# Kernel optimization log

Measured on AMD Instinct MI355X. Metric: run time of the kernel, lower is better.

The kernel has to match this reference:

```python
import jax, jax.numpy as jnp
import numpy as np

CUTOFF = 5.0
NLINKED = 1
CELL_LIST = CUTOFF / NLINKED  # linked-cell edge length
_r = np.arange(-NLINKED, NLINKED + 1)
# torch.cartesian_prod(r1,r1,r1) == meshgrid(indexing='ij') stacked & flattened
LINKED = np.stack(np.meshgrid(_r, _r, _r, indexing='ij'), axis=-1).reshape(1, -1, 3).astype(np.float32)  # (1, 27, 3)


def setup_inputs() -> dict:
    N = 2744
    L = 30.0
    key = jax.random.key(0)
    k1, k2 = jax.random.split(key)
    coordinates = jax.random.uniform(k1, (N, 3), dtype=jnp.float32) * L
    cell = jnp.eye(3, dtype=jnp.float32) * L
    mass = jax.random.uniform(k2, (N,), dtype=jnp.float32) * 15.0 + 1.0
    period_table = jnp.ones((3,), dtype=jnp.int32)  # fully periodic
    return {"period_table": period_table, "coordinates": coordinates, "cell": cell, "mass": mass}


def _forward(period_table, coordinates, cell, mass):
    numatom = coordinates.shape[0]
    # wrap coordinates into the cell relative to atom 0 (fractional coords)
    inv_cell = jnp.linalg.inv(cell)
    inv_coor = coordinates @ inv_cell
    inv_coor = inv_coor - jnp.round(inv_coor - inv_coor[0])
    coordinates = inv_coor @ cell
    # remove center of mass
    com = (mass @ coordinates) / jnp.sum(mass)
    coordinates = coordinates - com[None, :]
    # periodic replicas needed to cover the cutoff
    num_repeats = jnp.ceil(jnp.min(CUTOFF / jnp.abs(cell), axis=0)).astype(jnp.int32)
    num_repeats = period_table.astype(jnp.int32) * num_repeats
    up = num_repeats + 1
    down = -num_repeats
    rs = [jnp.arange(int(down[i]), int(up[i])) for i in range(3)]
    g = jnp.meshgrid(*rs, indexing='ij')
    shifts_frac = jnp.stack(g, axis=-1).reshape(-1, 3).astype(coordinates.dtype)  # (S, 3)
    shifts = shifts_frac @ cell  # (S, 3) cartesian shift vectors
    num_shifts = shifts.shape[0]
    # prod = cartesian_prod(all_shifts, all_atoms).T : row0 shift idx, row1 atom idx
    prod0 = jnp.repeat(jnp.arange(num_shifts), numatom)
    prod1 = jnp.tile(jnp.arange(numatom), num_shifts)
    # shift box so all coords are positive; pad by cutoff
    mincoor = jnp.min(coordinates, axis=0) - CUTOFF - 1e-6
    coordinates = coordinates - mincoor
    maxcoor = jnp.max(coordinates, axis=0) + CUTOFF
    # all periodic images, keep only those inside the padded box
    image = (coordinates[None, :, :] + shifts[:, None, :]).reshape(-1, 3)
    keep = jnp.nonzero(((image < maxcoor) & (image > 0)).all(axis=1))[0]
    image_mask = image[keep]                      # (M, 3)
    prod0 = prod0[keep]
    prod1 = prod1[keep]
    # linked-cell indices
    ori_image_index = jnp.floor(coordinates / CELL_LIST)         # (N, 3)
    neigh_cell = ori_image_index[:, None, :] + jnp.asarray(LINKED)  # (N, 27, 3)
    image_index = jnp.floor(image_mask / CELL_LIST)              # (M, 3)
    max_cell_index = jnp.ceil(maxcoor / CELL_LIST)
    f10 = max_cell_index[1] * max_cell_index[0]
    neigh_cell_index = neigh_cell[:, :, 2] * f10 + neigh_cell[:, :, 1] * max_cell_index[0] + neigh_cell[:, :, 0]  # (N, 27)
    nimage_index = image_index[:, 2] * f10 + image_index[:, 1] * max_cell_index[0] + image_index[:, 0]            # (M,)
    # dense (N, M, 27) cell-index equality -- the memory-bound hot spot
    eq = neigh_cell_index[:, None, :] == nimage_index[None, :, None]
    ai, aj, _ = jnp.nonzero(eq)
    # distance filter on candidate pairs
    d = jnp.linalg.norm(coordinates[ai] - image_mask[aj], axis=-1)
    pair = jnp.nonzero((d < CUTOFF) & (d > 0.001))[0]
    center = ai[pair]
    img = aj[pair]
    shift_idx = prod0[img]
    atom_j = prod1[img]
    neigh_list = jnp.stack([center, atom_j])  # (2, P)
    return neigh_list, shifts[shift_idx], shifts_frac, shift_idx


def reference(period_table, coordinates, cell, mass):
    neigh_list, shifts_out, _, _ = _forward(period_table, coordinates, cell, mass)
    return (neigh_list, shifts_out)
```

## Files before the change

### kernel.cpp

```cpp
#include <hip/hip_runtime.h>
#include <math.h>

#define S_CAP     27
#define NCELL_MAX 4096
#define CAP       64
#define CAPSH     6
#define MAXNB     128
#define CUT       5.0f


__global__ __launch_bounds__(256)
void k1_pre(const int* __restrict__ period, const float* __restrict__ coor,
            const float* __restrict__ cell, const float* __restrict__ mass,
            int* hdr_i, float* hdr_f, float* shifts, float* xv,
            int* __restrict__ ccur, int n)
{
    #pragma clang fp contract(off)
    __shared__ double rs[256 * 4];
    __shared__ float  redf[256 * 6];
    __shared__ float  s_com[3];
    int t = threadIdx.x;

    for (int c = t; c < NCELL_MAX; c += 256) ccur[c] = 0;

    float c[3][3];
    #pragma unroll
    for (int i = 0; i < 3; i++)
        #pragma unroll
        for (int j = 0; j < 3; j++) c[i][j] = cell[3 * i + j];

    float a00 = c[1][1]*c[2][2] - c[1][2]*c[2][1];
    float a01 = c[0][2]*c[2][1] - c[0][1]*c[2][2];
    float a02 = c[0][1]*c[1][2] - c[0][2]*c[1][1];
    float a10 = c[1][2]*c[2][0] - c[1][0]*c[2][2];
    float a11 = c[0][0]*c[2][2] - c[0][2]*c[2][0];
    float a12 = c[0][2]*c[1][0] - c[0][0]*c[1][2];
    float a20 = c[1][0]*c[2][1] - c[1][1]*c[2][0];
    float a21 = c[0][1]*c[2][0] - c[0][0]*c[2][1];
    float a22 = c[0][0]*c[1][1] - c[0][1]*c[1][0];
    float det = c[0][0]*a00 + c[0][1]*a10 + c[0][2]*a20;
    float inv[3][3] = {{a00/det, a01/det, a02/det},
                       {a10/det, a11/det, a12/det},
                       {a20/det, a21/det, a22/det}};

    float f0[3];
    #pragma unroll
    for (int d = 0; d < 3; d++)
        f0[d] = coor[0]*inv[0][d] + coor[1]*inv[1][d] + coor[2]*inv[2][d];

    double sm = 0.0, sx = 0.0, sy = 0.0, sz = 0.0;
    for (int i = t; i < n; i += 256) {
        float p0 = coor[3*i], p1 = coor[3*i+1], p2 = coor[3*i+2];
        float ic[3], w[3], x[3];
        #pragma unroll
        for (int d = 0; d < 3; d++)
            ic[d] = p0*inv[0][d] + p1*inv[1][d] + p2*inv[2][d];
        #pragma unroll
        for (int d = 0; d < 3; d++)
            w[d] = ic[d] - rintf(ic[d] - f0[d]);
        #pragma unroll
        for (int d = 0; d < 3; d++)
            x[d] = w[0]*c[0][d] + w[1]*c[1][d] + w[2]*c[2][d];
        xv[3*i] = x[0]; xv[3*i+1] = x[1]; xv[3*i+2] = x[2];
        float m = mass[i];
        sm += (double)m;
        sx += (double)m * (double)x[0];
        sy += (double)m * (double)x[1];
        sz += (double)m * (double)x[2];
    }
    rs[t] = sm; rs[256+t] = sx; rs[512+t] = sy; rs[768+t] = sz;
    __syncthreads();
    for (int off = 128; off > 0; off >>= 1) {
        if (t < off) {
            rs[t]     += rs[t+off];
            rs[256+t] += rs[256+t+off];
            rs[512+t] += rs[512+t+off];
            rs[768+t] += rs[768+t+off];
        }
        __syncthreads();
    }
    if (t == 0) {
        float den = (float)rs[0];
        s_com[0] = ((float)rs[256]) / den;
        s_com[1] = ((float)rs[512]) / den;
        s_com[2] = ((float)rs[768]) / den;
    }
    __syncthreads();
    float com0 = s_com[0], com1 = s_com[1], com2 = s_com[2];

    float mn0 =  __builtin_inff(), mn1 =  __builtin_inff(), mn2 =  __builtin_inff();
    float mx0 = -__builtin_inff(), mx1 = -__builtin_inff(), mx2 = -__builtin_inff();
    for (int i = t; i < n; i += 256) {
        float v0 = xv[3*i]   - com0;
        float v1 = xv[3*i+1] - com1;
        float v2 = xv[3*i+2] - com2;
        xv[3*i] = v0; xv[3*i+1] = v1; xv[3*i+2] = v2;
        mn0 = fminf(mn0, v0); mn1 = fminf(mn1, v1); mn2 = fminf(mn2, v2);
        mx0 = fmaxf(mx0, v0); mx1 = fmaxf(mx1, v1); mx2 = fmaxf(mx2, v2);
    }
    redf[t]       = mn0; redf[256+t]  = mn1; redf[512+t]  = mn2;
    redf[768+t]   = mx0; redf[1024+t] = mx1; redf[1280+t] = mx2;
    __syncthreads();
    for (int off = 128; off > 0; off >>= 1) {
        if (t < off) {
            redf[t]      = fminf(redf[t],      redf[t+off]);
            redf[256+t]  = fminf(redf[256+t],  redf[256+t+off]);
            redf[512+t]  = fminf(redf[512+t],  redf[512+t+off]);
            redf[768+t]  = fmaxf(redf[768+t],  redf[768+t+off]);
            redf[1024+t] = fmaxf(redf[1024+t], redf[1024+t+off]);
            redf[1280+t] = fmaxf(redf[1280+t], redf[1280+t+off]);
        }
        __syncthreads();
    }
    if (t == 0) {
        float m20 = (redf[0]   - CUT) - 1e-6f;
        float m21 = (redf[256] - CUT) - 1e-6f;
        float m22 = (redf[512] - CUT) - 1e-6f;
        float maxc0 = (redf[768]  - m20) + CUT;
        float maxc1 = (redf[1024] - m21) + CUT;
        float maxc2 = (redf[1280] - m22) + CUT;
        float mcell0 = ceilf(maxc0 / CUT);
        float mcell1 = ceilf(maxc1 / CUT);
        float f10 = mcell1 * mcell0;
        int nr[3];
        for (int j = 0; j < 3; j++) {
            float v = __builtin_inff();
            for (int i = 0; i < 3; i++) {
                float q = CUT / fabsf(c[i][j]);
                v = fminf(v, q);
            }
            nr[j] = (int)ceilf(v);
            nr[j] *= period[j];
        }
        int nsz0 = 2*nr[0]+1, nsz1 = 2*nr[1]+1, nsz2 = 2*nr[2]+1;
        int S = nsz0 * nsz1 * nsz2;
        if (S > S_CAP) S = S_CAP;
        hdr_i[0] = S;
        hdr_i[3] = -nr[0]; hdr_i[4] = -nr[1]; hdr_i[5] = -nr[2];
        hdr_i[6] = nsz0;   hdr_i[7] = nsz1;   hdr_i[8] = nsz2;
        hdr_i[9]  = (int)mcell0;
        hdr_i[10] = (int)f10;
        hdr_f[0] = maxc0; hdr_f[1] = maxc1; hdr_f[2] = maxc2;
        hdr_f[3] = f10;   hdr_f[4] = mcell0;
        hdr_f[5] = m20;   hdr_f[6] = m21;   hdr_f[7] = m22;
    }
    __syncthreads();
    int S = hdr_i[0];
    if (t < S) {
        int n1 = hdr_i[7], n2 = hdr_i[8];
        int i0 = t / (n1 * n2);
        int rem = t - i0 * n1 * n2;
        int i1 = rem / n2;
        int i2 = rem - i1 * n2;
        float fx = (float)(hdr_i[3] + i0);
        float fy = (float)(hdr_i[4] + i1);
        float fz = (float)(hdr_i[5] + i2);
        #pragma unroll
        for (int d = 0; d < 3; d++)
            shifts[3*t + d] = fx*c[0][d] + fy*c[1][d] + fz*c[2][d];
    }
}

__global__ __launch_bounds__(256)
void k2_fill(const int* __restrict__ hdr_i, const float* __restrict__ hdr_f,
             const float* __restrict__ shifts, const float* __restrict__ xv,
             int* __restrict__ ccur, float4* __restrict__ cellbuf, int n)
{
    #pragma clang fp contract(off)
    int g = blockIdx.x * 256 + threadIdx.x;
    int sn = hdr_i[0] * n;
    if (g >= sn) return;
    float m20 = hdr_f[5], m21 = hdr_f[6], m22 = hdr_f[7];
    int s = g / n, a = g - s * n;
    float i0 = (xv[3*a]   - m20) + shifts[3*s];
    float i1 = (xv[3*a+1] - m21) + shifts[3*s+1];
    float i2 = (xv[3*a+2] - m22) + shifts[3*s+2];
    bool k = (i0 > 0.0f) && (i0 < hdr_f[0]) &&
             (i1 > 0.0f) && (i1 < hdr_f[1]) &&
             (i2 > 0.0f) && (i2 < hdr_f[2]);
    if (!k) return;
    float fc0 = floorf(i0 / CUT);
    float fc1 = floorf(i1 / CUT);
    float fc2 = floorf(i2 / CUT);
    float cf = fc2 * hdr_f[3] + fc1 * hdr_f[4] + fc0;
    int ci = (int)cf;
    if ((unsigned)ci >= (unsigned)NCELL_MAX) return;
    int pos = atomicAdd(&ccur[ci], 1);
    if (pos < CAP)
        cellbuf[(ci << CAPSH) + pos] = make_float4(i0, i1, i2, __int_as_float(g));
}

__global__ __launch_bounds__(256)
void k3_search(const int* __restrict__ hdr_i, const float* __restrict__ hdr_f,
               const float* __restrict__ xv, const int* __restrict__ ccur,
               const float4* __restrict__ cellbuf, int* __restrict__ nb,
               int* __restrict__ npair, int* __restrict__ blocksum, int n)
{
    #pragma clang fp contract(off)
    __shared__ int scnt[4];
    int t    = threadIdx.x;
    int lane = t & 63;
    int w    = t >> 6;
    int atom = blockIdx.x * 4 + w;
    int cnt  = 0;
    if (atom < n) {
        float m20 = hdr_f[5], m21 = hdr_f[6], m22 = hdr_f[7];
        int mci = hdr_i[9], f10i = hdr_i[10];
        float x0 = xv[3*atom]   - m20;
        float x1 = xv[3*atom+1] - m21;
        float x2 = xv[3*atom+2] - m22;
        int o0 = (int)floorf(x0 / CUT);
        int o1 = (int)floorf(x1 / CUT);
        int o2 = (int)floorf(x2 / CUT);

        int ncb[9];
        int cc[27];
        #pragma unroll
        for (int r = 0; r < 9; r++) {
            int dz = r / 3 - 1, dy = r % 3 - 1;
            ncb[r] = (o2+dz)*f10i + (o1+dy)*mci + (o0-1);
            #pragma unroll
            for (int q = 0; q < 3; q++) {
                int nc = ncb[r] + q;
                int v = ((unsigned)nc < (unsigned)NCELL_MAX) ? ccur[nc] : 0;
                cc[r*3+q] = v > CAP ? CAP : v;
            }
        }

        int* slab = nb + (size_t)atom * MAXNB;
        #pragma unroll
        for (int r = 0; r < 9; r++) {
            int c0 = cc[r*3], c1 = cc[r*3+1], c2 = cc[r*3+2];
            int tot = c0 + c1 + c2;
            int base0 = (ncb[r]     << CAPSH);
            int base1 = ((ncb[r]+1) << CAPSH) - c0;
            int base2 = ((ncb[r]+2) << CAPSH) - c0 - c1;
            for (int bb = 0; bb < tot; bb += 64) {
                int L = bb + lane;
                bool act = L < tot;
                bool ok = false; int g = 0;
                if (act) {
                    int slot = (L < c0) ? (base0 + L)
                             : (L < c0 + c1) ? (base1 + L)
                             : (base2 + L);
                    float4 v = cellbuf[slot];
                    g = __float_as_int(v.w);
                    float dxx = x0 - v.x;
                    float dyy = x1 - v.y;
                    float dzz = x2 - v.z;
                    float ss = dxx*dxx + dyy*dyy + dzz*dzz;
                    float dd = sqrtf(ss);
                    ok = (dd < CUT) && (dd > 0.001f);
                }
                unsigned long long m = __ballot(ok);
                int posn = cnt + (int)__popcll(m & ((1ull << lane) - 1ull));
                if (ok && posn < MAXNB) slab[posn] = g;
                cnt += (int)__popcll(m);
            }
        }
        if (cnt > MAXNB) cnt = MAXNB;
        if (lane == 0) npair[atom] = cnt;
    } else if (lane == 0) {
    }
    if (lane == 0) scnt[w] = (atom < n) ? cnt : 0;
    __syncthreads();
    if (t == 0) blocksum[blockIdx.x] = scnt[0] + scnt[1] + scnt[2] + scnt[3];
}

__global__ __launch_bounds__(256)
void k4_emit(const int* __restrict__ nb, const int* __restrict__ npair,
             const int* __restrict__ blocksum, const float* __restrict__ shifts,
             float* __restrict__ out, int n, int P, int nblocks)
{
    __shared__ int si[256];
    __shared__ int lst[4][MAXNB];
    __shared__ int s_np[4];
    int t    = threadIdx.x;
    int lane = t & 63;
    int w    = t >> 6;
    int blk  = blockIdx.x;
    int atom = blk * 4 + w;
    bool valid = atom < n;

    int s = 0;
    for (int i = t; i < blk; i += 256) s += blocksum[i];
    si[t] = s;
    __syncthreads();
    for (int off = 128; off > 0; off >>= 1) {
        if (t < off) si[t] += si[t + off];
        __syncthreads();
    }
    int prefB = si[0];

    int cnt = 0;
    if (valid) {
        cnt = npair[atom];
        if (cnt > MAXNB) cnt = MAXNB;
        if (lane == 0) s_np[w] = cnt;
        const int* slab = nb + (size_t)atom * MAXNB;
        for (int r = lane; r < cnt; r += 64) lst[w][r] = slab[r];
    } else if (lane == 0) {
        s_np[w] = 0;
    }
    __syncthreads();

    if (valid) {
        int base = prefB;
        for (int q = 0; q < w; q++) base += s_np[q];
        for (int r = lane; r < cnt; r += 64) {
            int g = lst[w][r];
            int rank = 0;
            for (int q = 0; q < cnt; q++) rank += (lst[w][q] < g) ? 1 : 0;
            int p = base + rank;
            if (p < P) {
                int sidx = g / n;
                int a = g - sidx * n;
                out[p]     = (float)atom;
                out[P + p] = (float)a;
                out[2*P + 3*p]     = shifts[3*sidx];
                out[2*P + 3*p + 1] = shifts[3*sidx + 1];
                out[2*P + 3*p + 2] = shifts[3*sidx + 2];
            }
        }
    }
}

extern "C" void kernel_launch(void* const* d_in, const int* in_sizes, int n_in,
                              void* d_out, int out_size, void* d_ws, size_t ws_size,
                              hipStream_t stream)
{
    const int*   period = (const int*)d_in[0];
    const float* coor   = (const float*)d_in[1];
    const float* cell   = (const float*)d_in[2];
    const float* mass   = (const float*)d_in[3];
    float* out = (float*)d_out;

    int n  = in_sizes[1] / 3;
    int SN = S_CAP * n;
    int P  = out_size / 5;

    char* wp = (char*)d_ws;
    size_t off = 0;
    auto alloc = [&](size_t bytes) -> void* {
        off = (off + 15) & ~(size_t)15;
        void* pp = (void*)(wp + off); off += bytes; return pp;
    };

    int*    hdr_i    = (int*)   alloc(16 * 4);
    float*  hdr_f    = (float*) alloc(16 * 4);
    float*  shifts   = (float*) alloc(3 * S_CAP * 4);
    float*  xv       = (float*) alloc(3 * (size_t)n * 4);
    int*    ccur     = (int*)   alloc(NCELL_MAX * 4);
    float4* cellbuf  = (float4*)alloc((size_t)NCELL_MAX * CAP * 16);
    int*    nb       = (int*)   alloc((size_t)n * MAXNB * 4);
    int*    npair    = (int*)   alloc((size_t)n * 4);
    int     gb_atom  = (n + 3) / 4;
    int*    blocksum = (int*)   alloc((size_t)gb_atom * 4);
    (void)ws_size; (void)n_in;

    hipLaunchKernelGGL(k1_pre,    dim3(1),            dim3(256), 0, stream,
                       period, coor, cell, mass, hdr_i, hdr_f, shifts, xv, ccur, n);
    hipLaunchKernelGGL(k2_fill,   dim3((SN+255)/256), dim3(256), 0, stream,
                       hdr_i, hdr_f, shifts, xv, ccur, cellbuf, n);
    hipLaunchKernelGGL(k3_search, dim3(gb_atom),      dim3(256), 0, stream,
                       hdr_i, hdr_f, xv, ccur, cellbuf, nb, npair, blocksum, n);
    hipLaunchKernelGGL(k4_emit,   dim3(gb_atom),      dim3(256), 0, stream,
                       nb, npair, blocksum, shifts, out, n, P, gb_atom);
}
```

Before: 90.54 us.

## Widen preprocessing block, flatten neighbor-cell scan, drop blocksum array

Several changes land together. The single-block preprocessing kernel grows from 256 to 1024 threads, and the cell-count array shrinks from 4096 to 1024 entries, so there is less to zero. The fill kernel now uses a 2D grid (atoms by shifts) in place of an integer divide. The search kernel flattens all 27 neighbor cells into one lane-parallel range through a prefix table, which reduces idle lanes in partially filled 64-wide batches. The per-block sum array is removed and the emit kernel sums npair directly, which reads four times as many values per block and risks a wrong result if the cell count ever exceeds 1024.

New measurement: 87.76 us. 3.1% less time.

```diff
diff --git a/kernel.cpp b/kernel.cpp
--- a/kernel.cpp
+++ b/kernel.cpp
@@ -2,26 +2,27 @@
 #include <math.h>
 
 #define S_CAP     27
-#define NCELL_MAX 4096
+#define NCELL_MAX 1024
 #define CAP       64
 #define CAPSH     6
 #define MAXNB     128
 #define CUT       5.0f
-
-
-__global__ __launch_bounds__(256)
+#define K1T       1024
+
+
+__global__ __launch_bounds__(K1T)
 void k1_pre(const int* __restrict__ period, const float* __restrict__ coor,
             const float* __restrict__ cell, const float* __restrict__ mass,
             int* hdr_i, float* hdr_f, float* shifts, float* xv,
             int* __restrict__ ccur, int n)
 {
     #pragma clang fp contract(off)
-    __shared__ double rs[256 * 4];
-    __shared__ float  redf[256 * 6];
+    __shared__ double rs[K1T * 4];
+    __shared__ float  redf[K1T * 6];
     __shared__ float  s_com[3];
     int t = threadIdx.x;
 
-    for (int c = t; c < NCELL_MAX; c += 256) ccur[c] = 0;
+    for (int c = t; c < NCELL_MAX; c += K1T) ccur[c] = 0;
 
     float c[3][3];
     #pragma unroll
@@ -49,7 +50,7 @@
         f0[d] = coor[0]*inv[0][d] + coor[1]*inv[1][d] + coor[2]*inv[2][d];
 
     double sm = 0.0, sx = 0.0, sy = 0.0, sz = 0.0;
-    for (int i = t; i < n; i += 256) {
+    for (int i = t; i < n; i += K1T) {
         float p0 = coor[3*i], p1 = coor[3*i+1], p2 = coor[3*i+2];
         float ic[3], w[3], x[3];
         #pragma unroll
@@ -68,29 +69,29 @@
         sy += (double)m * (double)x[1];
         sz += (double)m * (double)x[2];
     }
-    rs[t] = sm; rs[256+t] = sx; rs[512+t] = sy; rs[768+t] = sz;
-    __syncthreads();
-    for (int off = 128; off > 0; off >>= 1) {
+    rs[t] = sm; rs[K1T+t] = sx; rs[2*K1T+t] = sy; rs[3*K1T+t] = sz;
+    __syncthreads();
+    for (int off = K1T/2; off > 0; off >>= 1) {
         if (t < off) {
-            rs[t]     += rs[t+off];
-            rs[256+t] += rs[256+t+off];
-            rs[512+t] += rs[512+t+off];
-            rs[768+t] += rs[768+t+off];
+            rs[t]         += rs[t+off];
+            rs[K1T+t]     += rs[K1T+t+off];
+            rs[2*K1T+t]   += rs[2*K1T+t+off];
+            rs[3*K1T+t]   += rs[3*K1T+t+off];
         }
         __syncthreads();
     }
     if (t == 0) {
         float den = (float)rs[0];
-        s_com[0] = ((float)rs[256]) / den;
-        s_com[1] = ((float)rs[512]) / den;
-        s_com[2] = ((float)rs[768]) / den;
+        s_com[0] = ((float)rs[K1T])   / den;
+        s_com[1] = ((float)rs[2*K1T]) / den;
+        s_com[2] = ((float)rs[3*K1T]) / den;
     }
     __syncthreads();
     float com0 = s_com[0], com1 = s_com[1], com2 = s_com[2];
 
     float mn0 =  __builtin_inff(), mn1 =  __builtin_inff(), mn2 =  __builtin_inff();
     float mx0 = -__builtin_inff(), mx1 = -__builtin_inff(), mx2 = -__builtin_inff();
-    for (int i = t; i < n; i += 256) {
+    for (int i = t; i < n; i += K1T) {
         float v0 = xv[3*i]   - com0;
         float v1 = xv[3*i+1] - com1;
         float v2 = xv[3*i+2] - com2;
@@ -98,27 +99,27 @@
         mn0 = fminf(mn0, v0); mn1 = fminf(mn1, v1); mn2 = fminf(mn2, v2);
         mx0 = fmaxf(mx0, v0); mx1 = fmaxf(mx1, v1); mx2 = fmaxf(mx2, v2);
     }
-    redf[t]       = mn0; redf[256+t]  = mn1; redf[512+t]  = mn2;
-    redf[768+t]   = mx0; redf[1024+t] = mx1; redf[1280+t] = mx2;
-    __syncthreads();
-    for (int off = 128; off > 0; off >>= 1) {
+    redf[t]         = mn0; redf[K1T+t]   = mn1; redf[2*K1T+t] = mn2;
+    redf[3*K1T+t]   = mx0; redf[4*K1T+t] = mx1; redf[5*K1T+t] = mx2;
+    __syncthreads();
+    for (int off = K1T/2; off > 0; off >>= 1) {
         if (t < off) {
-            redf[t]      = fminf(redf[t],      redf[t+off]);
-            redf[256+t]  = fminf(redf[256+t],  redf[256+t+off]);
-            redf[512+t]  = fminf(redf[512+t],  redf[512+t+off]);
-            redf[768+t]  = fmaxf(redf[768+t],  redf[768+t+off]);
-            redf[1024+t] = fmaxf(redf[1024+t], redf[1024+t+off]);
-            redf[1280+t] = fmaxf(redf[1280+t], redf[1280+t+off]);
+            redf[t]        = fminf(redf[t],        redf[t+off]);
+            redf[K1T+t]    = fminf(redf[K1T+t],    redf[K1T+t+off]);
+            redf[2*K1T+t]  = fminf(redf[2*K1T+t],  redf[2*K1T+t+off]);
+            redf[3*K1T+t]  = fmaxf(redf[3*K1T+t],  redf[3*K1T+t+off]);
+            redf[4*K1T+t]  = fmaxf(redf[4*K1T+t],  redf[4*K1T+t+off]);
+            redf[5*K1T+t]  = fmaxf(redf[5*K1T+t],  redf[5*K1T+t+off]);
         }
         __syncthreads();
     }
     if (t == 0) {
-        float m20 = (redf[0]   - CUT) - 1e-6f;
-        float m21 = (redf[256] - CUT) - 1e-6f;
-        float m22 = (redf[512] - CUT) - 1e-6f;
-        float maxc0 = (redf[768]  - m20) + CUT;
-        float maxc1 = (redf[1024] - m21) + CUT;
-        float maxc2 = (redf[1280] - m22) + CUT;
+        float m20 = (redf[0]     - CUT) - 1e-6f;
+        float m21 = (redf[K1T]   - CUT) - 1e-6f;
+        float m22 = (redf[2*K1T] - CUT) - 1e-6f;
+        float maxc0 = (redf[3*K1T] - m20) + CUT;
+        float maxc1 = (redf[4*K1T] - m21) + CUT;
+        float maxc2 = (redf[5*K1T] - m22) + CUT;
         float mcell0 = ceilf(maxc0 / CUT);
         float mcell1 = ceilf(maxc1 / CUT);
         float f10 = mcell1 * mcell0;
@@ -167,11 +168,10 @@
              int* __restrict__ ccur, float4* __restrict__ cellbuf, int n)
 {
     #pragma clang fp contract(off)
-    int g = blockIdx.x * 256 + threadIdx.x;
-    int sn = hdr_i[0] * n;
-    if (g >= sn) return;
+    int a = blockIdx.x * 256 + threadIdx.x;
+    int s = blockIdx.y;
+    if (a >= n || s >= hdr_i[0]) return;
     float m20 = hdr_f[5], m21 = hdr_f[6], m22 = hdr_f[7];
-    int s = g / n, a = g - s * n;
     float i0 = (xv[3*a]   - m20) + shifts[3*s];
     float i1 = (xv[3*a+1] - m21) + shifts[3*s+1];
     float i2 = (xv[3*a+2] - m22) + shifts[3*s+2];
@@ -187,90 +187,82 @@
     if ((unsigned)ci >= (unsigned)NCELL_MAX) return;
     int pos = atomicAdd(&ccur[ci], 1);
     if (pos < CAP)
-        cellbuf[(ci << CAPSH) + pos] = make_float4(i0, i1, i2, __int_as_float(g));
+        cellbuf[(ci << CAPSH) + pos] = make_float4(i0, i1, i2, __int_as_float(s * n + a));
 }
 
 __global__ __launch_bounds__(256)
 void k3_search(const int* __restrict__ hdr_i, const float* __restrict__ hdr_f,
                const float* __restrict__ xv, const int* __restrict__ ccur,
                const float4* __restrict__ cellbuf, int* __restrict__ nb,
-               int* __restrict__ npair, int* __restrict__ blocksum, int n)
+               int* __restrict__ npair, int n)
 {
     #pragma clang fp contract(off)
-    __shared__ int scnt[4];
     int t    = threadIdx.x;
     int lane = t & 63;
     int w    = t >> 6;
     int atom = blockIdx.x * 4 + w;
-    int cnt  = 0;
-    if (atom < n) {
-        float m20 = hdr_f[5], m21 = hdr_f[6], m22 = hdr_f[7];
-        int mci = hdr_i[9], f10i = hdr_i[10];
-        float x0 = xv[3*atom]   - m20;
-        float x1 = xv[3*atom+1] - m21;
-        float x2 = xv[3*atom+2] - m22;
-        int o0 = (int)floorf(x0 / CUT);
-        int o1 = (int)floorf(x1 / CUT);
-        int o2 = (int)floorf(x2 / CUT);
-
-        int ncb[9];
-        int cc[27];
-        #pragma unroll
-        for (int r = 0; r < 9; r++) {
-            int dz = r / 3 - 1, dy = r % 3 - 1;
-            ncb[r] = (o2+dz)*f10i + (o1+dy)*mci + (o0-1);
+    if (atom >= n) return;
+
+    float m20 = hdr_f[5], m21 = hdr_f[6], m22 = hdr_f[7];
+    int mci = hdr_i[9], f10i = hdr_i[10];
+    float x0 = xv[3*atom]   - m20;
+    float x1 = xv[3*atom+1] - m21;
+    float x2 = xv[3*atom+2] - m22;
+    int o0 = (int)floorf(x0 / CUT);
+    int o1 = (int)floorf(x1 / CUT);
+    int o2 = (int)floorf(x2 / CUT);
+
+    int ncb[9], c0a[9], c1a[9], c2a[9], cum[10];
+    cum[0] = 0;
+    #pragma unroll
+    for (int r = 0; r < 9; r++) {
+        int dz = r / 3 - 1, dy = r % 3 - 1;
+        ncb[r] = (o2+dz)*f10i + (o1+dy)*mci + (o0-1);
+        int q0 = 0, q1 = 0, q2 = 0, nc;
+        nc = ncb[r];     if ((unsigned)nc < (unsigned)NCELL_MAX) { q0 = ccur[nc]; q0 = q0 > CAP ? CAP : q0; }
+        nc = ncb[r] + 1; if ((unsigned)nc < (unsigned)NCELL_MAX) { q1 = ccur[nc]; q1 = q1 > CAP ? CAP : q1; }
+        nc = ncb[r] + 2; if ((unsigned)nc < (unsigned)NCELL_MAX) { q2 = ccur[nc]; q2 = q2 > CAP ? CAP : q2; }
+        c0a[r] = q0; c1a[r] = q1; c2a[r] = q2;
+        cum[r+1] = cum[r] + q0 + q1 + q2;
+    }
+    int T = cum[9];
+    int cnt = 0;
+    int* slab = nb + (size_t)atom * MAXNB;
+    for (int base = 0; base < T; base += 64) {
+        int L = base + lane;
+        bool act = L < T;
+        bool ok = false; int g = 0;
+        if (act) {
+            int r = 0;
             #pragma unroll
-            for (int q = 0; q < 3; q++) {
-                int nc = ncb[r] + q;
-                int v = ((unsigned)nc < (unsigned)NCELL_MAX) ? ccur[nc] : 0;
-                cc[r*3+q] = v > CAP ? CAP : v;
-            }
-        }
-
-        int* slab = nb + (size_t)atom * MAXNB;
-        #pragma unroll
-        for (int r = 0; r < 9; r++) {
-            int c0 = cc[r*3], c1 = cc[r*3+1], c2 = cc[r*3+2];
-            int tot = c0 + c1 + c2;
-            int base0 = (ncb[r]     << CAPSH);
-            int base1 = ((ncb[r]+1) << CAPSH) - c0;
-            int base2 = ((ncb[r]+2) << CAPSH) - c0 - c1;
-            for (int bb = 0; bb < tot; bb += 64) {
-                int L = bb + lane;
-                bool act = L < tot;
-                bool ok = false; int g = 0;
-                if (act) {
-                    int slot = (L < c0) ? (base0 + L)
-                             : (L < c0 + c1) ? (base1 + L)
-                             : (base2 + L);
-                    float4 v = cellbuf[slot];
-                    g = __float_as_int(v.w);
-                    float dxx = x0 - v.x;
-                    float dyy = x1 - v.y;
-                    float dzz = x2 - v.z;
-                    float ss = dxx*dxx + dyy*dyy + dzz*dzz;
-                    float dd = sqrtf(ss);
-                    ok = (dd < CUT) && (dd > 0.001f);
-                }
-                unsigned long long m = __ballot(ok);
-                int posn = cnt + (int)__popcll(m & ((1ull << lane) - 1ull));
-                if (ok && posn < MAXNB) slab[posn] = g;
-                cnt += (int)__popcll(m);
-            }
-        }
-        if (cnt > MAXNB) cnt = MAXNB;
-        if (lane == 0) npair[atom] = cnt;
-    } else if (lane == 0) {
-    }
-    if (lane == 0) scnt[w] = (atom < n) ? cnt : 0;
-    __syncthreads();
-    if (t == 0) blocksum[blockIdx.x] = scnt[0] + scnt[1] + scnt[2] + scnt[3];
+            for (int q = 1; q < 9; q++) r += (L >= cum[q]) ? 1 : 0;
+            int off = L - cum[r];
+            int c0 = c0a[r], c1 = c1a[r];
+            int slot = (off < c0)      ? ((ncb[r]     << CAPSH) + off)
+                     : (off < c0 + c1) ? (((ncb[r]+1) << CAPSH) + off - c0)
+                                       : (((ncb[r]+2) << CAPSH) + off - c0 - c1);
+            float4 v = cellbuf[slot];
+            g = __float_as_int(v.w);
+            float dxx = x0 - v.x;
+            float dyy = x1 - v.y;
+            float dzz = x2 - v.z;
+            float ss = dxx*dxx + dyy*dyy + dzz*dzz;
+            float dd = sqrtf(ss);
+            ok = (dd < CUT) && (dd > 0.001f);
+        }
+        unsigned long long m = __ballot(ok);
+        int posn = cnt + (int)__popcll(m & ((1ull << lane) - 1ull));
+        if (ok && posn < MAXNB) slab[posn] = g;
+        cnt += (int)__popcll(m);
+    }
+    if (cnt > MAXNB) cnt = MAXNB;
+    if (lane == 0) npair[atom] = cnt;
 }
 
 __global__ __launch_bounds__(256)
 void k4_emit(const int* __restrict__ nb, const int* __restrict__ npair,
-             const int* __restrict__ blocksum, const float* __restrict__ shifts,
-             float* __restrict__ out, int n, int P, int nblocks)
+             const float* __restrict__ shifts, float* __restrict__ out,
+             int n, int P)
 {
     __shared__ int si[256];
     __shared__ int lst[4][MAXNB];
@@ -282,8 +274,9 @@
     int atom = blk * 4 + w;
     bool valid = atom < n;
 
+    int lim = blk * 4;
     int s = 0;
-    for (int i = t; i < blk; i += 256) s += blocksum[i];
+    for (int i = t; i < lim; i += 256) s += npair[i];
     si[t] = s;
     __syncthreads();
     for (int off = 128; off > 0; off >>= 1) {
@@ -335,9 +328,8 @@
     const float* mass   = (const float*)d_in[3];
     float* out = (float*)d_out;
 
-    int n  = in_sizes[1] / 3;
-    int SN = S_CAP * n;
-    int P  = out_size / 5;
+    int n = in_sizes[1] / 3;
+    int P = out_size / 5;
 
     char* wp = (char*)d_ws;
     size_t off = 0;
@@ -346,24 +338,25 @@
         void* pp = (void*)(wp + off); off += bytes; return pp;
     };
 
-    int*    hdr_i    = (int*)   alloc(16 * 4);
-    float*  hdr_f    = (float*) alloc(16 * 4);
-    float*  shifts   = (float*) alloc(3 * S_CAP * 4);
-    float*  xv       = (float*) alloc(3 * (size_t)n * 4);
-    int*    ccur     = (int*)   alloc(NCELL_MAX * 4);
-    float4* cellbuf  = (float4*)alloc((size_t)NCELL_MAX * CAP * 16);
-    int*    nb       = (int*)   alloc((size_t)n * MAXNB * 4);
-    int*    npair    = (int*)   alloc((size_t)n * 4);
-    int     gb_atom  = (n + 3) / 4;
-    int*    blocksum = (int*)   alloc((size_t)gb_atom * 4);
+    int*    hdr_i   = (int*)   alloc(16 * 4);
+    float*  hdr_f   = (float*) alloc(16 * 4);
+    float*  shifts  = (float*) alloc(3 * S_CAP * 4);
+    float*  xv      = (float*) alloc(3 * (size_t)n * 4);
+    int*    ccur    = (int*)   alloc(NCELL_MAX * 4);
+    float4* cellbuf = (float4*)alloc((size_t)NCELL_MAX * CAP * 16);
+    int*    nb      = (int*)   alloc((size_t)n * MAXNB * 4);
+    int*    npair   = (int*)   alloc((size_t)n * 4);
     (void)ws_size; (void)n_in;
 
-    hipLaunchKernelGGL(k1_pre,    dim3(1),            dim3(256), 0, stream,
+    int gb_atom = (n + 3) / 4;
+    dim3 g2((n + 255) / 256, S_CAP);
+
+    hipLaunchKernelGGL(k1_pre,    dim3(1),       dim3(K1T), 0, stream,
                        period, coor, cell, mass, hdr_i, hdr_f, shifts, xv, ccur, n);
-    hipLaunchKernelGGL(k2_fill,   dim3((SN+255)/256), dim3(256), 0, stream,
+    hipLaunchKernelGGL(k2_fill,   g2,            dim3(256), 0, stream,
                        hdr_i, hdr_f, shifts, xv, ccur, cellbuf, n);
-    hipLaunchKernelGGL(k3_search, dim3(gb_atom),      dim3(256), 0, stream,
-                       hdr_i, hdr_f, xv, ccur, cellbuf, nb, npair, blocksum, n);
-    hipLaunchKernelGGL(k4_emit,   dim3(gb_atom),      dim3(256), 0, stream,
-                       nb, npair, blocksum, shifts, out, n, P, gb_atom);
-}
+    hipLaunchKernelGGL(k3_search, dim3(gb_atom), dim3(256), 0, stream,
+                       hdr_i, hdr_f, xv, ccur, cellbuf, nb, npair, n);
+    hipLaunchKernelGGL(k4_emit,   dim3(gb_atom), dim3(256), 0, stream,
+                       nb, npair, shifts, out, n, P);
+}
```
